# Kernel optimization log

Hardware: AMD Instinct MI355X
Metric: run time of the kernel (lower is better)

Reference implementation:

```python
import jax, jax.numpy as jnp
import numpy as np

N = 100000
E = 3200000
C = 32

def setup_inputs() -> dict:
    key = jax.random.key(0)
    k1, k2, k3, k4 = jax.random.split(key, 4)
    adj = jax.random.uniform(k1, (E,), dtype=jnp.float32)          # per-edge weights
    labels = jax.random.uniform(k2, (N, C), dtype=jnp.float32)     # node label distributions
    src = jax.random.randint(k3, (E,), 0, N, dtype=jnp.int64)
    dst = jax.random.randint(k4, (E,), 0, N, dtype=jnp.int64)
    return {"adj": adj, "labels": labels, "src": src, "dst": dst, "n_lpa": 3}

def reference(adj, labels, src, dst, n_lpa):
    # One hop of label propagation: msg_e = label[src_e] * w_e; out_v = sum_{e: dst_e=v} msg_e
    n_nodes = labels.shape[0]

    def lp(lab):
        msg = lab[src] * adj[:, None]                 # [E, C] gather-multiply
        return jax.ops.segment_sum(msg, dst, num_segments=n_nodes)  # scatter-sum over dst

    # soft_label == 0 path of the original forward: plain iterated propagation
    for _ in range(n_lpa):
        labels = lp(labels)
    return labels
```

## Files before the change

kernel.cpp:

```cpp
#include <hip/hip_runtime.h>
#include <hip/hip_bf16.h>


#define LPA_C   32
#define BKT_LG  7
#define BKT_NV  (1 << BKT_LG)
#define CHUNK   6400

__global__ __launch_bounds__(512)
void k_histA(const int* __restrict__ dst, int* __restrict__ C,
             int E, int P, int nbkt) {
    __shared__ int h[1024];
    int c = blockIdx.x;
    int base = c * CHUNK;
    int lim = min(CHUNK, E - base);
    for (int i = threadIdx.x; i < nbkt; i += 512) h[i] = 0;
    __syncthreads();
    for (int i = threadIdx.x; i < lim; i += 512)
        atomicAdd(&h[dst[base + i] >> BKT_LG], 1);
    __syncthreads();
    for (int i = threadIdx.x; i < nbkt; i += 512) C[i * P + c] = h[i];
}

__global__ __launch_bounds__(512)
void k_scanC(int* __restrict__ C, int* __restrict__ btot, int P) {
    __shared__ int s[512];
    int b = blockIdx.x;
    int t = threadIdx.x;
    int v = (t < P) ? C[b * P + t] : 0;
    s[t] = v;
    __syncthreads();
    for (int off = 1; off < 512; off <<= 1) {
        int x = (t >= off) ? s[t - off] : 0;
        __syncthreads();
        s[t] += x;
        __syncthreads();
    }
    if (t < P) C[b * P + t] = s[t] - v;
    if (t == 511) btot[b] = s[511];
}

__global__ __launch_bounds__(1024)
void k_scanB(const int* __restrict__ btot, int* __restrict__ bstart,
             int* __restrict__ row_start, int nb, int N, int E) {
    __shared__ int s[1024];
    int t = threadIdx.x;
    int v = (t < nb) ? btot[t] : 0;
    s[t] = v;
    __syncthreads();
    for (int off = 1; off < 1024; off <<= 1) {
        int x = (t >= off) ? s[t - off] : 0;
        __syncthreads();
        s[t] += x;
        __syncthreads();
    }
    if (t < nb) bstart[t] = s[t] - v;
    if (t == 0) { bstart[nb] = E; row_start[N] = E; }
}

__global__ __launch_bounds__(512)
void k_scatA(const int* __restrict__ src, const int* __restrict__ dst,
             const float* __restrict__ adj, const int* __restrict__ C,
             const int* __restrict__ bstart, int2* __restrict__ mid,
             int E, int P, int nbkt) {
    __shared__ int2 sedge[CHUNK];
    __shared__ int  lofs[1025];
    __shared__ int  cur[1024];
    __shared__ int  s2[512];
    int c = blockIdx.x;
    int base = c * CHUNK;
    int lim = min(CHUNK, E - base);
    int t = threadIdx.x;

    for (int i = t; i < nbkt; i += 512) cur[i] = 0;
    __syncthreads();
    for (int i = t; i < lim; i += 512)
        atomicAdd(&cur[dst[base + i] >> BKT_LG], 1);
    __syncthreads();

    int k0 = 2 * t, k1 = 2 * t + 1;
    int a0 = (k0 < nbkt) ? cur[k0] : 0;
    int a1 = (k1 < nbkt) ? cur[k1] : 0;
    int ts = a0 + a1;
    s2[t] = ts;
    __syncthreads();
    for (int off = 1; off < 512; off <<= 1) {
        int x = (t >= off) ? s2[t - off] : 0;
        __syncthreads();
        s2[t] += x;
        __syncthreads();
    }
    int pre = s2[t] - ts;
    if (k0 < nbkt) lofs[k0] = pre;
    if (k1 < nbkt) lofs[k1] = pre + a0;
    if (t == 0) lofs[nbkt] = lim;
    __syncthreads();
    for (int i = t; i < nbkt; i += 512) cur[i] = lofs[i];
    __syncthreads();

    for (int i = t; i < lim; i += 512) {
        int d = dst[base + i];
        int b = d >> BKT_LG;
        int pos = atomicAdd(&cur[b], 1);
        sedge[pos] = make_int2(src[base + i] | ((d & (BKT_NV - 1)) << 20),
                               __float_as_int(adj[base + i]));
    }
    __syncthreads();

    for (int i = t; i < lim; i += 512) {
        int lo = 0, hi = nbkt;
        while (hi - lo > 1) {
            int m = (lo + hi) >> 1;
            if (lofs[m] <= i) lo = m; else hi = m;
        }
        int gdst = bstart[lo] + C[lo * P + c] + (i - lofs[lo]);
        mid[gdst] = sedge[i];
    }
}

__global__ __launch_bounds__(512)
void k_sortnode(const int2* __restrict__ mid, const int* __restrict__ bstart,
                int2* __restrict__ edges, int* __restrict__ row_start, int N) {
    __shared__ int lcnt[BKT_NV];
    __shared__ int lofs[BKT_NV];
    int b = blockIdx.x;
    int s0 = bstart[b], e0 = bstart[b + 1];
    int v0 = b << BKT_LG;
    int nv = min(BKT_NV, N - v0);

    if (threadIdx.x < BKT_NV) lcnt[threadIdx.x] = 0;
    __syncthreads();
    for (int i = s0 + threadIdx.x; i < e0; i += 512)
        atomicAdd(&lcnt[mid[i].x >> 20], 1);
    __syncthreads();
    if (threadIdx.x < BKT_NV) lofs[threadIdx.x] = lcnt[threadIdx.x];
    __syncthreads();
    for (int off = 1; off < BKT_NV; off <<= 1) {
        int x = 0;
        if (threadIdx.x < BKT_NV && threadIdx.x >= off) x = lofs[threadIdx.x - off];
        __syncthreads();
        if (threadIdx.x < BKT_NV) lofs[threadIdx.x] += x;
        __syncthreads();
    }
    if (threadIdx.x < BKT_NV) {
        int base = s0 + lofs[threadIdx.x] - lcnt[threadIdx.x];
        lcnt[threadIdx.x] = base;
        if (threadIdx.x < nv) row_start[v0 + threadIdx.x] = base;
    }
    __syncthreads();
    for (int i = s0 + threadIdx.x; i < e0; i += 512) {
        int2 ed = mid[i];
        int pos = atomicAdd(&lcnt[ed.x >> 20], 1);
        edges[pos] = make_int2(ed.x & 0xFFFFF, ed.y);
    }
}

__global__ void k_tobf16(const float* __restrict__ in, ushort* __restrict__ out, int n) {
    int i = blockIdx.x * blockDim.x + threadIdx.x;
    if (i < n) out[i] = __bfloat16_as_ushort(__float2bfloat16(in[i]));
}

template <int OUT16>
__global__ void lpa_pull16(const int2* __restrict__ edges,
                           const int* __restrict__ row_start,
                           const ushort* __restrict__ lab_in,
                           void* __restrict__ out_v, int N) {
    int node = blockIdx.x * 8 + (threadIdx.x >> 5);
    int c = threadIdx.x & 31;
    if (node >= N) return;
    int j = row_start[node];
    int end = row_start[node + 1];
    float acc0 = 0.f, acc1 = 0.f, acc2 = 0.f, acc3 = 0.f;
#define GATH(S) (__uint_as_float((unsigned)lab_in[((size_t)(unsigned)(S) << 5) + c] << 16))
    for (; j + 16 <= end; j += 16) {
        int4 q0 = *(const int4*)(edges + j);
        int4 q1 = *(const int4*)(edges + j + 2);
        int4 q2 = *(const int4*)(edges + j + 4);
        int4 q3 = *(const int4*)(edges + j + 6);
        int4 q4 = *(const int4*)(edges + j + 8);
        int4 q5 = *(const int4*)(edges + j + 10);
        int4 q6 = *(const int4*)(edges + j + 12);
        int4 q7 = *(const int4*)(edges + j + 14);
        acc0 += __int_as_float(q0.y) * GATH(q0.x);
        acc1 += __int_as_float(q0.w) * GATH(q0.z);
        acc2 += __int_as_float(q1.y) * GATH(q1.x);
        acc3 += __int_as_float(q1.w) * GATH(q1.z);
        acc0 += __int_as_float(q2.y) * GATH(q2.x);
        acc1 += __int_as_float(q2.w) * GATH(q2.z);
        acc2 += __int_as_float(q3.y) * GATH(q3.x);
        acc3 += __int_as_float(q3.w) * GATH(q3.z);
        acc0 += __int_as_float(q4.y) * GATH(q4.x);
        acc1 += __int_as_float(q4.w) * GATH(q4.z);
        acc2 += __int_as_float(q5.y) * GATH(q5.x);
        acc3 += __int_as_float(q5.w) * GATH(q5.z);
        acc0 += __int_as_float(q6.y) * GATH(q6.x);
        acc1 += __int_as_float(q6.w) * GATH(q6.z);
        acc2 += __int_as_float(q7.y) * GATH(q7.x);
        acc3 += __int_as_float(q7.w) * GATH(q7.z);
    }
    for (; j + 8 <= end; j += 8) {
        int4 q0 = *(const int4*)(edges + j);
        int4 q1 = *(const int4*)(edges + j + 2);
        int4 q2 = *(const int4*)(edges + j + 4);
        int4 q3 = *(const int4*)(edges + j + 6);
        acc0 += __int_as_float(q0.y) * GATH(q0.x);
        acc1 += __int_as_float(q0.w) * GATH(q0.z);
        acc2 += __int_as_float(q1.y) * GATH(q1.x);
        acc3 += __int_as_float(q1.w) * GATH(q1.z);
        acc0 += __int_as_float(q2.y) * GATH(q2.x);
        acc1 += __int_as_float(q2.w) * GATH(q2.z);
        acc2 += __int_as_float(q3.y) * GATH(q3.x);
        acc3 += __int_as_float(q3.w) * GATH(q3.z);
    }
    for (; j < end; ++j) {
        int2 e = edges[j];
        acc0 += __int_as_float(e.y) * GATH(e.x);
    }
#undef GATH
    float acc = (acc0 + acc1) + (acc2 + acc3);
    if (OUT16) {
        ((ushort*)out_v)[((size_t)node << 5) + c] =
            __bfloat16_as_ushort(__float2bfloat16(acc));
    } else {
        ((float*)out_v)[((size_t)node << 5) + c] = acc;
    }
}

__global__ void lpa_scatter_fb(const float* __restrict__ adj,
                               const float* __restrict__ lab_in,
                               const int* __restrict__ src,
                               const int* __restrict__ dst,
                               float* __restrict__ out, int E) {
    long long idx = (long long)blockIdx.x * blockDim.x + threadIdx.x;
    int e = (int)(idx >> 5);
    if (e >= E) return;
    int c = (int)(idx & 31);
    float v = lab_in[(long long)src[e] * LPA_C + c] * adj[e];
    unsafeAtomicAdd(&out[(long long)dst[e] * LPA_C + c], v);
}

extern "C" void kernel_launch(void* const* d_in, const int* in_sizes, int n_in,
                              void* d_out, int out_size, void* d_ws, size_t ws_size,
                              hipStream_t stream) {
    const float* adj    = (const float*)d_in[0];
    const float* labels = (const float*)d_in[1];
    const int*   src    = (const int*)d_in[2];
    const int*   dst    = (const int*)d_in[3];

    const int E  = in_sizes[0];
    const int NC = in_sizes[1];
    const int N  = NC / LPA_C;
    const int NBKT = (N + BKT_NV - 1) >> BKT_LG;
    const int P  = (E + CHUNK - 1) / CHUNK;
    float* out = (float*)d_out;

    char* p = (char*)d_ws;
    int2*  edges     = (int2*)p;  p += (size_t)E * sizeof(int2);
    int2*  mid       = (int2*)p;  p += (size_t)E * sizeof(int2);
    int*   C         = (int*)p;   p += (size_t)NBKT * P * sizeof(int);
    int*   btot      = (int*)p;   p += (size_t)NBKT * sizeof(int);
    int*   bstart    = (int*)p;   p += (size_t)(NBKT + 1) * sizeof(int);
    int*   row_start = (int*)p;   p += (size_t)(N + 1) * sizeof(int);
    size_t needed = (size_t)(p - (char*)d_ws);
    ushort* lab16_a = (ushort*)mid;
    ushort* lab16_b = (ushort*)mid + (size_t)NC;

    if (ws_size < needed || NBKT > 1024 || P > 512 || N >= (1 << 20)) {
        float* ws0 = (float*)d_ws;
        const size_t nbytes = (size_t)NC * sizeof(float);
        const long long total = (long long)E * LPA_C;
        const unsigned grid = (unsigned)((total + 255) / 256);
        hipMemsetAsync(out, 0, nbytes, stream);
        lpa_scatter_fb<<<grid, 256, 0, stream>>>(adj, labels, src, dst, out, E);
        hipMemsetAsync(ws0, 0, nbytes, stream);
        lpa_scatter_fb<<<grid, 256, 0, stream>>>(adj, out, src, dst, ws0, E);
        hipMemsetAsync(out, 0, nbytes, stream);
        lpa_scatter_fb<<<grid, 256, 0, stream>>>(adj, ws0, src, dst, out, E);
        return;
    }

    k_histA   <<<P, 512, 0, stream>>>(dst, C, E, P, NBKT);
    k_scanC   <<<NBKT, 512, 0, stream>>>(C, btot, P);
    k_scanB   <<<1, 1024, 0, stream>>>(btot, bstart, row_start, NBKT, N, E);
    k_scatA   <<<P, 512, 0, stream>>>(src, dst, adj, C, bstart, mid, E, P, NBKT);
    k_sortnode<<<NBKT, 512, 0, stream>>>(mid, bstart, edges, row_start, N);

    k_tobf16<<<(NC + 255) / 256, 256, 0, stream>>>(labels, lab16_a, NC);

    const unsigned gridN = (unsigned)((N + 7) / 8);
    lpa_pull16<1><<<gridN, 256, 0, stream>>>(edges, row_start, lab16_a, lab16_b, N);
    lpa_pull16<1><<<gridN, 256, 0, stream>>>(edges, row_start, lab16_b, lab16_a, N);
    lpa_pull16<0><<<gridN, 256, 0, stream>>>(edges, row_start, lab16_a, out, N);
}
```

Before: 248.4 us.

## Split each propagation hop into two source-half passes for L2 locality

Within each destination node, edges are now sorted by whether the source index falls in the lower or upper half of the nodes, with a new row_mid array marking the split. Each hop runs as two pull kernels: the first gathers only from lower-half sources and writes an fp32 partial into the output buffer, and the second adds upper-half contributions and writes the result. The aim is to halve the gathered label working set per kernel so it fits in L2. In exchange it adds extra partial-sum read and write traffic and three more kernel launches.

```diff
diff --git a/kernel.cpp b/kernel.cpp
--- a/kernel.cpp
+++ b/kernel.cpp
@@ -120,37 +120,47 @@
 
 __global__ __launch_bounds__(512)
 void k_sortnode(const int2* __restrict__ mid, const int* __restrict__ bstart,
-                int2* __restrict__ edges, int* __restrict__ row_start, int N) {
-    __shared__ int lcnt[BKT_NV];
-    __shared__ int lofs[BKT_NV];
+                int2* __restrict__ edges, int* __restrict__ row_start,
+                int* __restrict__ row_mid, int N, int HALF) {
+    __shared__ int kcnt[2 * BKT_NV];
+    __shared__ int kofs[2 * BKT_NV];
     int b = blockIdx.x;
     int s0 = bstart[b], e0 = bstart[b + 1];
     int v0 = b << BKT_LG;
     int nv = min(BKT_NV, N - v0);
-
-    if (threadIdx.x < BKT_NV) lcnt[threadIdx.x] = 0;
-    __syncthreads();
-    for (int i = s0 + threadIdx.x; i < e0; i += 512)
-        atomicAdd(&lcnt[mid[i].x >> 20], 1);
-    __syncthreads();
-    if (threadIdx.x < BKT_NV) lofs[threadIdx.x] = lcnt[threadIdx.x];
-    __syncthreads();
-    for (int off = 1; off < BKT_NV; off <<= 1) {
+    int t = threadIdx.x;
+
+    if (t < 2 * BKT_NV) kcnt[t] = 0;
+    __syncthreads();
+    for (int i = s0 + t; i < e0; i += 512) {
+        int x = mid[i].x;
+        int key = ((x >> 20) << 1) | (((x & 0xFFFFF) >= HALF) ? 1 : 0);
+        atomicAdd(&kcnt[key], 1);
+    }
+    __syncthreads();
+    if (t < 2 * BKT_NV) kofs[t] = kcnt[t];
+    __syncthreads();
+    for (int off = 1; off < 2 * BKT_NV; off <<= 1) {
         int x = 0;
-        if (threadIdx.x < BKT_NV && threadIdx.x >= off) x = lofs[threadIdx.x - off];
-        __syncthreads();
-        if (threadIdx.x < BKT_NV) lofs[threadIdx.x] += x;
-        __syncthreads();
-    }
-    if (threadIdx.x < BKT_NV) {
-        int base = s0 + lofs[threadIdx.x] - lcnt[threadIdx.x];
-        lcnt[threadIdx.x] = base;
-        if (threadIdx.x < nv) row_start[v0 + threadIdx.x] = base;
-    }
-    __syncthreads();
-    for (int i = s0 + threadIdx.x; i < e0; i += 512) {
+        if (t < 2 * BKT_NV && t >= off) x = kofs[t - off];
+        __syncthreads();
+        if (t < 2 * BKT_NV) kofs[t] += x;
+        __syncthreads();
+    }
+    if (t < 2 * BKT_NV) {
+        int excl = s0 + kofs[t] - kcnt[t];
+        kcnt[t] = excl;
+        int local = t >> 1;
+        if (local < nv) {
+            if ((t & 1) == 0) row_start[v0 + local] = excl;
+            else              row_mid[v0 + local]  = excl;
+        }
+    }
+    __syncthreads();
+    for (int i = s0 + t; i < e0; i += 512) {
         int2 ed = mid[i];
-        int pos = atomicAdd(&lcnt[ed.x >> 20], 1);
+        int key = ((ed.x >> 20) << 1) | (((ed.x & 0xFFFFF) >= HALF) ? 1 : 0);
+        int pos = atomicAdd(&kcnt[key], 1);
         edges[pos] = make_int2(ed.x & 0xFFFFF, ed.y);
     }
 }
@@ -160,17 +170,27 @@
     if (i < n) out[i] = __bfloat16_as_ushort(__float2bfloat16(in[i]));
 }
 
-template <int OUT16>
+template <int PASS, int OUT16>
 __global__ void lpa_pull16(const int2* __restrict__ edges,
                            const int* __restrict__ row_start,
+                           const int* __restrict__ row_mid,
                            const ushort* __restrict__ lab_in,
+                           float* __restrict__ partial,
                            void* __restrict__ out_v, int N) {
     int node = blockIdx.x * 8 + (threadIdx.x >> 5);
     int c = threadIdx.x & 31;
     if (node >= N) return;
-    int j = row_start[node];
-    int end = row_start[node + 1];
-    float acc0 = 0.f, acc1 = 0.f, acc2 = 0.f, acc3 = 0.f;
+    int j, end;
+    float acc0, acc1 = 0.f, acc2 = 0.f, acc3 = 0.f;
+    if (PASS == 0) {
+        j = row_start[node];
+        end = row_mid[node];
+        acc0 = 0.f;
+    } else {
+        j = row_mid[node];
+        end = row_start[node + 1];
+        acc0 = partial[((size_t)node << 5) + c];
+    }
 #define GATH(S) (__uint_as_float((unsigned)lab_in[((size_t)(unsigned)(S) << 5) + c] << 16))
     for (; j + 16 <= end; j += 16) {
         int4 q0 = *(const int4*)(edges + j);
@@ -218,7 +238,9 @@
     }
 #undef GATH
     float acc = (acc0 + acc1) + (acc2 + acc3);
-    if (OUT16) {
+    if (PASS == 0) {
+        partial[((size_t)node << 5) + c] = acc;
+    } else if (OUT16) {
         ((ushort*)out_v)[((size_t)node << 5) + c] =
             __bfloat16_as_ushort(__float2bfloat16(acc));
     } else {
@@ -250,6 +272,7 @@
     const int E  = in_sizes[0];
     const int NC = in_sizes[1];
     const int N  = NC / LPA_C;
+    const int HALF = (N + 1) / 2;
     const int NBKT = (N + BKT_NV - 1) >> BKT_LG;
     const int P  = (E + CHUNK - 1) / CHUNK;
     float* out = (float*)d_out;
@@ -261,9 +284,11 @@
     int*   btot      = (int*)p;   p += (size_t)NBKT * sizeof(int);
     int*   bstart    = (int*)p;   p += (size_t)(NBKT + 1) * sizeof(int);
     int*   row_start = (int*)p;   p += (size_t)(N + 1) * sizeof(int);
+    int*   row_mid   = (int*)p;   p += (size_t)N * sizeof(int);
     size_t needed = (size_t)(p - (char*)d_ws);
     ushort* lab16_a = (ushort*)mid;
     ushort* lab16_b = (ushort*)mid + (size_t)NC;
+    float* partial = out;
 
     if (ws_size < needed || NBKT > 1024 || P > 512 || N >= (1 << 20)) {
         float* ws0 = (float*)d_ws;
@@ -283,12 +308,22 @@
     k_scanC   <<<NBKT, 512, 0, stream>>>(C, btot, P);
     k_scanB   <<<1, 1024, 0, stream>>>(btot, bstart, row_start, NBKT, N, E);
     k_scatA   <<<P, 512, 0, stream>>>(src, dst, adj, C, bstart, mid, E, P, NBKT);
-    k_sortnode<<<NBKT, 512, 0, stream>>>(mid, bstart, edges, row_start, N);
+    k_sortnode<<<NBKT, 512, 0, stream>>>(mid, bstart, edges, row_start, row_mid,
+                                         N, HALF);
 
     k_tobf16<<<(NC + 255) / 256, 256, 0, stream>>>(labels, lab16_a, NC);
 
     const unsigned gridN = (unsigned)((N + 7) / 8);
-    lpa_pull16<1><<<gridN, 256, 0, stream>>>(edges, row_start, lab16_a, lab16_b, N);
-    lpa_pull16<1><<<gridN, 256, 0, stream>>>(edges, row_start, lab16_b, lab16_a, N);
-    lpa_pull16<0><<<gridN, 256, 0, stream>>>(edges, row_start, lab16_a, out, N);
-}
+    lpa_pull16<0, 0><<<gridN, 256, 0, stream>>>(edges, row_start, row_mid,
+                                                lab16_a, partial, nullptr, N);
+    lpa_pull16<1, 1><<<gridN, 256, 0, stream>>>(edges, row_start, row_mid,
+                                                lab16_a, partial, lab16_b, N);
+    lpa_pull16<0, 0><<<gridN, 256, 0, stream>>>(edges, row_start, row_mid,
+                                                lab16_b, partial, nullptr, N);
+    lpa_pull16<1, 1><<<gridN, 256, 0, stream>>>(edges, row_start, row_mid,
+                                                lab16_b, partial, lab16_a, N);
+    lpa_pull16<0, 0><<<gridN, 256, 0, stream>>>(edges, row_start, row_mid,
+                                                lab16_a, partial, nullptr, N);
+    lpa_pull16<1, 0><<<gridN, 256, 0, stream>>>(edges, row_start, row_mid,
+                                                lab16_a, partial, out, N);
+}
```

Measured after the change: 329.2 us. +32.5%, slower.
